# Kernel tuning notes

Measured on AMD Instinct MI355X. Metric: run time of the kernel, lower is better.

The kernel has to match this reference:

```python
import jax, jax.numpy as jnp
import numpy as np

N_NODES = 131072
N_EDGES = 1048576
D_IN, D_HID, D_OUT = 64, 64, 3
NUM_GRAPHS = 32


def setup_inputs() -> dict:
    key = jax.random.key(0)
    k = jax.random.split(key, 6)
    x = jax.random.normal(k[0], (N_NODES, D_IN), dtype=jnp.float32)
    edge_index = jax.random.randint(k[1], (2, N_EDGES), 0, N_NODES, dtype=jnp.int64)
    # batch assignment: 32 graphs of 4096 contiguous nodes each
    batch = jnp.repeat(jnp.arange(NUM_GRAPHS, dtype=jnp.int32), N_NODES // NUM_GRAPHS)
    W1 = jax.random.normal(k[2], (D_IN, D_HID), dtype=jnp.float32) * (1.0 / np.sqrt(D_IN))
    b1 = jnp.zeros((D_HID,), dtype=jnp.float32)
    W2 = jax.random.normal(k[3], (D_HID, D_OUT), dtype=jnp.float32) * (1.0 / np.sqrt(D_HID))
    b2 = jnp.zeros((D_OUT,), dtype=jnp.float32)
    return {"x": x, "edge_index": edge_index, "batch": batch,
            "W1": W1, "b1": b1, "W2": W2, "b2": b2}


def _gcn_conv(x, W, b, row, col, deg_inv_sqrt):
    # PyG GCNConv: x' = D^{-1/2}(A+I)D^{-1/2} X W + b (self-loops added)
    h = x @ W  # [N, d_out]
    norm = deg_inv_sqrt[row] * deg_inv_sqrt[col]  # [E]
    msg = h[row] * norm[:, None]                  # gather + scale
    agg = jax.ops.segment_sum(msg, col, num_segments=x.shape[0])
    # self-loop contribution: norm_ii = deg_inv_sqrt[i]^2
    agg = agg + h * (deg_inv_sqrt * deg_inv_sqrt)[:, None]
    return agg + b


def reference(x, edge_index, batch, W1, b1, W2, b2):
    N = x.shape[0]
    row, col = edge_index[0], edge_index[1]
    # degree at target nodes, including self-loops (+1)
    ones = jnp.ones((row.shape[0],), dtype=x.dtype)
    deg = jax.ops.segment_sum(ones, col, num_segments=N) + 1.0
    deg_inv_sqrt = jax.lax.rsqrt(deg)

    h = _gcn_conv(x, W1, b1, row, col, deg_inv_sqrt)
    h = jax.nn.relu(h)
    # F.dropout in eval mode is identity
    h = _gcn_conv(h, W2, b2, row, col, deg_inv_sqrt)

    # global_mean_pool over batch vector
    batch = batch.astype(jnp.int32)
    sums = jax.ops.segment_sum(h, batch, num_segments=NUM_GRAPHS)
    counts = jax.ops.segment_sum(jnp.ones((N,), dtype=h.dtype), batch, num_segments=NUM_GRAPHS)
    return sums / jnp.maximum(counts, 1.0)[:, None]
```

## Files before the change

### kernel.cpp

```cpp
#include <hip/hip_runtime.h>

#define NN 131072
#define NE 1048576
#define DD 64
#define NG 32
#define NPG 4096
#define NB 512
#define CAPB 2560
#define SCB 512

typedef __attribute__((ext_vector_type(2))) float f32x2;

extern "C" __global__ __launch_bounds__(256) void k_scgemm(
    const int* __restrict__ row, const int* __restrict__ col, int* __restrict__ bcursor,
    int* __restrict__ ebuf, const float* __restrict__ x, const float* __restrict__ W1,
    unsigned char* __restrict__ h1f, const float* __restrict__ b2, float* __restrict__ out) {
  __shared__ float4 wl[DD * 16];
  int t = threadIdx.x;
  if (blockIdx.x < SCB) {
    int* sh = reinterpret_cast<int*>(wl);
    int* sb = sh + NB;
    sh[t] = 0; sh[t + 256] = 0;
    __syncthreads();
    const int4* c4 = reinterpret_cast<const int4*>(col + blockIdx.x * 2048 + t * 8);
    int4 ca = c4[0], cb = c4[1];
    int cols[8] = {ca.x, ca.y, ca.z, ca.w, cb.x, cb.y, cb.z, cb.w};
    int lr[8];
#pragma unroll
    for (int k = 0; k < 8; ++k) lr[k] = atomicAdd(&sh[cols[k] >> 8], 1);
    __syncthreads();
    int h0 = sh[t];
    sb[t] = t * CAPB + (h0 ? atomicAdd(&bcursor[t], h0) : 0);
    int h1 = sh[t + 256];
    sb[t + 256] = (t + 256) * CAPB + (h1 ? atomicAdd(&bcursor[t + 256], h1) : 0);
    __syncthreads();
    const int4* r4 = reinterpret_cast<const int4*>(row + blockIdx.x * 2048 + t * 8);
    int4 ra = r4[0], rb = r4[1];
    int rows[8] = {ra.x, ra.y, ra.z, ra.w, rb.x, rb.y, rb.z, rb.w};
#pragma unroll
    for (int k = 0; k < 8; ++k) {
      int key = cols[k] >> 8;
      int pos = sb[key] + lr[k];
      if (pos < (key + 1) * CAPB)
        ebuf[pos] = (rows[k] << 8) | (cols[k] & 255);
    }
  } else {
    int gb = blockIdx.x - SCB;
    if (gb == 0 && t < NG * 3) out[t] = b2[t % 3];
    for (int i = t; i < DD * 16; i += 256) wl[i] = reinterpret_cast<const float4*>(W1)[i];
    __syncthreads();
    int jc = t & 3;
    int rg = t >> 2;
    size_t rbase = (size_t)gb * 128 + (size_t)rg * 2;
    const float4* xp = reinterpret_cast<const float4*>(x + rbase * DD);
    float4 acc[2][4];
#pragma unroll
    for (int r = 0; r < 2; ++r)
#pragma unroll
      for (int j = 0; j < 4; ++j) acc[r][j] = make_float4(0.f, 0.f, 0.f, 0.f);
#pragma unroll 2
    for (int kk = 0; kk < 16; ++kk) {
      float4 a0 = xp[kk];
      float4 a1 = xp[16 + kk];
#pragma unroll
      for (int j = 0; j < 4; ++j) {
        float4 w0 = wl[(4 * kk + 0) * 16 + jc * 4 + j];
        float4 w1 = wl[(4 * kk + 1) * 16 + jc * 4 + j];
        float4 w2 = wl[(4 * kk + 2) * 16 + jc * 4 + j];
        float4 w3 = wl[(4 * kk + 3) * 16 + jc * 4 + j];
        acc[0][j].x += a0.x * w0.x + a0.y * w1.x + a0.z * w2.x + a0.w * w3.x;
        acc[0][j].y += a0.x * w0.y + a0.y * w1.y + a0.z * w2.y + a0.w * w3.y;
        acc[0][j].z += a0.x * w0.z + a0.y * w1.z + a0.z * w2.z + a0.w * w3.z;
        acc[0][j].w += a0.x * w0.w + a0.y * w1.w + a0.z * w2.w + a0.w * w3.w;
        acc[1][j].x += a1.x * w0.x + a1.y * w1.x + a1.z * w2.x + a1.w * w3.x;
        acc[1][j].y += a1.x * w0.y + a1.y * w1.y + a1.z * w2.y + a1.w * w3.y;
        acc[1][j].z += a1.x * w0.z + a1.y * w1.z + a1.z * w2.z + a1.w * w3.z;
        acc[1][j].w += a1.x * w0.w + a1.y * w1.w + a1.z * w2.w + a1.w * w3.w;
      }
    }
#pragma unroll
    for (int r = 0; r < 2; ++r) {
      unsigned int d[4];
#pragma unroll
      for (int j = 0; j < 4; ++j) {
        float4 a = acc[r][j];
        int dj = __builtin_amdgcn_cvt_pk_fp8_f32(a.x, a.y, 0, false);
        dj = __builtin_amdgcn_cvt_pk_fp8_f32(a.z, a.w, dj, true);
        d[j] = (unsigned int)dj;
      }
      *reinterpret_cast<uint4*>(h1f + (rbase + r) * 64 + jc * 16) =
          make_uint4(d[0], d[1], d[2], d[3]);
    }
  }
}

extern "C" __global__ __launch_bounds__(256) void k_blocal(
    const int* __restrict__ ebuf, const int* __restrict__ bcursor, int* __restrict__ cnt,
    float* __restrict__ dis, int* __restrict__ starts, int* __restrict__ nbr) {
  __shared__ int sh[256];
  __shared__ int sx[256];
  int b = blockIdx.x, t = threadIdx.x;
  int bs = b * CAPB;
  int n_e = bcursor[b];
  if (n_e > CAPB) n_e = CAPB;
  sh[t] = 0;
  __syncthreads();
  for (int i = t; i < n_e; i += 256) atomicAdd(&sh[ebuf[bs + i] & 255], 1);
  __syncthreads();
  int v = sh[t];
  sx[t] = v;
  __syncthreads();
  for (int off = 1; off < 256; off <<= 1) {
    int u = (t >= off) ? sx[t - off] : 0;
    __syncthreads();
    sx[t] += u;
    __syncthreads();
  }
  int st = bs + sx[t] - v;
  int node = b * 256 + t;
  cnt[node] = v;
  dis[node] = rsqrtf((float)v + 1.0f);
  starts[node] = st;
  sx[t] = st;
  __syncthreads();
  for (int i = t; i < n_e; i += 256) {
    int ed = ebuf[bs + i];
    int pos = atomicAdd(&sx[ed & 255], 1);
    nbr[pos] = ed >> 8;
  }
}

extern "C" __global__ __launch_bounds__(256) void k_agg1f(
    const unsigned char* __restrict__ h1f, const int* __restrict__ starts,
    const int* __restrict__ cnt, const int* __restrict__ nbr, const float* __restrict__ dis,
    const float* __restrict__ b1, const float* __restrict__ W2, float4* __restrict__ h2) {
  __shared__ int2 sed[4][4][16];
  int lane = threadIdx.x & 63;
  int wid = threadIdx.x >> 6;
  int g = lane >> 4;
  int sl = lane & 15;
  int node = blockIdx.x * 16 + wid * 4 + g;
  int start = starts[node];
  int deg = cnt[node];
  float dc = dis[node];
  int2 s = make_int2(node, 0);
  if (sl < deg) {
    int nb = nbr[start + sl];
    s = make_int2(nb, __float_as_int(dis[nb] * dc));
  } else if (sl == deg) {
    s = make_int2(node, __float_as_int(dc * dc));
  }
  sed[wid][g][sl] = s;
  int m = (deg < 16) ? (deg + 1) : 16;
  int mw = max(m, __shfl_xor(m, 16));
  mw = max(mw, __shfl_xor(mw, 32));
  int mw8 = (mw + 7) & ~7;
  asm volatile("s_waitcnt lgkmcnt(0)" ::: "memory");
  __builtin_amdgcn_sched_barrier(0);
  const unsigned int* h1u = reinterpret_cast<const unsigned int*>(h1f);
  const int2* sp = sed[wid][g];
  float a0 = 0.f, a1 = 0.f, a2 = 0.f, a3 = 0.f;
  for (int e = 0; e < mw8; e += 8) {
    int2 e0 = sp[e + 0], e1 = sp[e + 1], e2 = sp[e + 2], e3 = sp[e + 3];
    int2 e4 = sp[e + 4], e5 = sp[e + 5], e6 = sp[e + 6], e7 = sp[e + 7];
    unsigned int u0 = h1u[(size_t)e0.x * 16 + sl];
    unsigned int u1 = h1u[(size_t)e1.x * 16 + sl];
    unsigned int u2 = h1u[(size_t)e2.x * 16 + sl];
    unsigned int u3 = h1u[(size_t)e3.x * 16 + sl];
    unsigned int u4 = h1u[(size_t)e4.x * 16 + sl];
    unsigned int u5 = h1u[(size_t)e5.x * 16 + sl];
    unsigned int u6 = h1u[(size_t)e6.x * 16 + sl];
    unsigned int u7 = h1u[(size_t)e7.x * 16 + sl];
    float w0 = __int_as_float(e0.y), w1 = __int_as_float(e1.y);
    float w2 = __int_as_float(e2.y), w3 = __int_as_float(e3.y);
    float w4 = __int_as_float(e4.y), w5 = __int_as_float(e5.y);
    float w6 = __int_as_float(e6.y), w7 = __int_as_float(e7.y);
    f32x2 p0 = __builtin_amdgcn_cvt_pk_f32_fp8(u0, false);
    f32x2 q0 = __builtin_amdgcn_cvt_pk_f32_fp8(u0, true);
    f32x2 p1 = __builtin_amdgcn_cvt_pk_f32_fp8(u1, false);
    f32x2 q1 = __builtin_amdgcn_cvt_pk_f32_fp8(u1, true);
    f32x2 p2 = __builtin_amdgcn_cvt_pk_f32_fp8(u2, false);
    f32x2 q2 = __builtin_amdgcn_cvt_pk_f32_fp8(u2, true);
    f32x2 p3 = __builtin_amdgcn_cvt_pk_f32_fp8(u3, false);
    f32x2 q3 = __builtin_amdgcn_cvt_pk_f32_fp8(u3, true);
    f32x2 p4 = __builtin_amdgcn_cvt_pk_f32_fp8(u4, false);
    f32x2 q4 = __builtin_amdgcn_cvt_pk_f32_fp8(u4, true);
    f32x2 p5 = __builtin_amdgcn_cvt_pk_f32_fp8(u5, false);
    f32x2 q5 = __builtin_amdgcn_cvt_pk_f32_fp8(u5, true);
    f32x2 p6 = __builtin_amdgcn_cvt_pk_f32_fp8(u6, false);
    f32x2 q6 = __builtin_amdgcn_cvt_pk_f32_fp8(u6, true);
    f32x2 p7 = __builtin_amdgcn_cvt_pk_f32_fp8(u7, false);
    f32x2 q7 = __builtin_amdgcn_cvt_pk_f32_fp8(u7, true);
    a0 = fmaf(w0, p0.x, a0); a1 = fmaf(w0, p0.y, a1); a2 = fmaf(w0, q0.x, a2); a3 = fmaf(w0, q0.y, a3);
    a0 = fmaf(w1, p1.x, a0); a1 = fmaf(w1, p1.y, a1); a2 = fmaf(w1, q1.x, a2); a3 = fmaf(w1, q1.y, a3);
    a0 = fmaf(w2, p2.x, a0); a1 = fmaf(w2, p2.y, a1); a2 = fmaf(w2, q2.x, a2); a3 = fmaf(w2, q2.y, a3);
    a0 = fmaf(w3, p3.x, a0); a1 = fmaf(w3, p3.y, a1); a2 = fmaf(w3, q3.x, a2); a3 = fmaf(w3, q3.y, a3);
    a0 = fmaf(w4, p4.x, a0); a1 = fmaf(w4, p4.y, a1); a2 = fmaf(w4, q4.x, a2); a3 = fmaf(w4, q4.y, a3);
    a0 = fmaf(w5, p5.x, a0); a1 = fmaf(w5, p5.y, a1); a2 = fmaf(w5, q5.x, a2); a3 = fmaf(w5, q5.y, a3);
    a0 = fmaf(w6, p6.x, a0); a1 = fmaf(w6, p6.y, a1); a2 = fmaf(w6, q6.x, a2); a3 = fmaf(w6, q6.y, a3);
    a0 = fmaf(w7, p7.x, a0); a1 = fmaf(w7, p7.y, a1); a2 = fmaf(w7, q7.x, a2); a3 = fmaf(w7, q7.y, a3);
  }
  if (deg >= 16) {
    for (int eo = 16; eo < deg; ++eo) {
      int r = nbr[start + eo];
      float q = dis[r] * dc;
      unsigned int u = h1u[(size_t)r * 16 + sl];
      f32x2 p = __builtin_amdgcn_cvt_pk_f32_fp8(u, false);
      f32x2 qq = __builtin_amdgcn_cvt_pk_f32_fp8(u, true);
      a0 = fmaf(q, p.x, a0); a1 = fmaf(q, p.y, a1);
      a2 = fmaf(q, qq.x, a2); a3 = fmaf(q, qq.y, a3);
    }
    float q = dc * dc;
    unsigned int u = h1u[(size_t)node * 16 + sl];
    f32x2 p = __builtin_amdgcn_cvt_pk_f32_fp8(u, false);
    f32x2 qq = __builtin_amdgcn_cvt_pk_f32_fp8(u, true);
    a0 = fmaf(q, p.x, a0); a1 = fmaf(q, p.y, a1);
    a2 = fmaf(q, qq.x, a2); a3 = fmaf(q, qq.y, a3);
  }
  float4 bb = *reinterpret_cast<const float4*>(b1 + 4 * sl);
  float z0 = fmaxf(a0 + bb.x, 0.f);
  float z1 = fmaxf(a1 + bb.y, 0.f);
  float z2 = fmaxf(a2 + bb.z, 0.f);
  float z3 = fmaxf(a3 + bb.w, 0.f);
  const float4* wp = reinterpret_cast<const float4*>(W2 + 12 * sl);
  float4 wA = wp[0];
  float4 wB = wp[1];
  float4 wC = wp[2];
  float v0 = z0 * wA.x + z1 * wA.w + z2 * wB.z + z3 * wC.y;
  float v1 = z0 * wA.y + z1 * wB.x + z2 * wB.w + z3 * wC.z;
  float v2 = z0 * wA.z + z1 * wB.y + z2 * wC.x + z3 * wC.w;
#pragma unroll
  for (int off = 8; off > 0; off >>= 1) {
    v0 += __shfl_xor(v0, off);
    v1 += __shfl_xor(v1, off);
    v2 += __shfl_xor(v2, off);
  }
  if (sl == 0) h2[node] = make_float4(v0 * dc, v1 * dc, v2 * dc, dc);
}

extern "C" __global__ __launch_bounds__(256) void k_agg2pool(
    const float4* __restrict__ h2, const int* __restrict__ starts, const int* __restrict__ cnt,
    const int* __restrict__ nbr, float* __restrict__ out) {
  int n = blockIdx.x * 256 + threadIdx.x;
  int start = starts[n], deg = cnt[n], end = start + deg;
  float4 hs = h2[n];
  float s0 = hs.x, s1 = hs.y, s2 = hs.z;
  int e = start;
  for (; e + 4 <= end; e += 4) {
    int n0 = nbr[e], n1 = nbr[e + 1], n2 = nbr[e + 2], n3 = nbr[e + 3];
    float4 h0 = h2[n0], h1 = h2[n1], g2 = h2[n2], g3 = h2[n3];
    s0 += (h0.x + h1.x) + (g2.x + g3.x);
    s1 += (h0.y + h1.y) + (g2.y + g3.y);
    s2 += (h0.z + h1.z) + (g2.z + g3.z);
  }
  for (; e < end; ++e) {
    float4 h0 = h2[nbr[e]];
    s0 += h0.x;
    s1 += h0.y;
    s2 += h0.z;
  }
  float dn = hs.w;
  s0 *= dn; s1 *= dn; s2 *= dn;
  __shared__ float red[3][256];
  int t = threadIdx.x;
  red[0][t] = s0; red[1][t] = s1; red[2][t] = s2;
  __syncthreads();
  for (int off = 128; off > 0; off >>= 1) {
    if (t < off) {
      red[0][t] += red[0][t + off];
      red[1][t] += red[1][t + off];
      red[2][t] += red[2][t + off];
    }
    __syncthreads();
  }
  if (t == 0) {
    int g = blockIdx.x >> 4;
    const float inv = 1.0f / (float)NPG;
    atomicAdd(&out[g * 3 + 0], red[0][0] * inv);
    atomicAdd(&out[g * 3 + 1], red[1][0] * inv);
    atomicAdd(&out[g * 3 + 2], red[2][0] * inv);
  }
}

extern "C" void kernel_launch(void* const* d_in, const int* in_sizes, int n_in,
                              void* d_out, int out_size, void* d_ws, size_t ws_size,
                              hipStream_t stream) {
  const float* x  = (const float*)d_in[0];
  const int*   ei = (const int*)d_in[1];
  const float* W1 = (const float*)d_in[3];
  const float* b1 = (const float*)d_in[4];
  const float* W2 = (const float*)d_in[5];
  const float* b2 = (const float*)d_in[6];
  const int* row = ei;
  const int* col = ei + NE;
  float* out = (float*)d_out;

  char* ws = (char*)d_ws;
  int*   cnt     = (int*)(ws + 0);
  float* dis     = (float*)(ws + (1u << 19));
  int*   starts  = (int*)(ws + (2u << 19));
  int*   bcursor = (int*)(ws + (3u << 19));
  int*   ebuf    = (int*)(ws + (4u << 19));
  int*   nbr     = (int*)(ws + (1u << 23));
  unsigned char* h1f = (unsigned char*)(ws + (1u << 24));
  float4* h2     = (float4*)(ws + (1u << 25) + 4096u);

  hipMemsetAsync(bcursor, 0, NB * sizeof(int), stream);
  k_scgemm<<<SCB + NN / 128, 256, 0, stream>>>(row, col, bcursor, ebuf, x, W1, h1f, b2, out);
  k_blocal<<<NB, 256, 0, stream>>>(ebuf, bcursor, cnt, dis, starts, nbr);
  k_agg1f<<<NN / 16, 256, 0, stream>>>(h1f, starts, cnt, nbr, dis, b1, W2, h2);
  k_agg2pool<<<NN / 256, 256, 0, stream>>>(h2, starts, cnt, nbr, out);
}
```

Measured before the change: 91.71 us.

## Split fused scatter/GEMM kernel, cache edges in LDS, two threads per node in pool

Splits the fused scatter+GEMM launch into a separate bucket-scatter kernel that handles 16 edges per thread and a standalone GEMM kernel that computes 4 rows per thread. The local bucket sort now keeps edges in shared memory so ebuf is read from global memory only once. The final aggregation+pool kernel assigns two threads per node, interleaving edges and combining them with a shuffle, to expose more memory parallelism. The cost is an extra kernel launch and the loss of the scatter/GEMM overlap the fused launch provided, plus higher register pressure in the GEMM.

```diff
diff --git a/kernel.cpp b/kernel.cpp
--- a/kernel.cpp
+++ b/kernel.cpp
@@ -7,96 +7,48 @@
 #define NPG 4096
 #define NB 512
 #define CAPB 2560
-#define SCB 512
 
 typedef __attribute__((ext_vector_type(2))) float f32x2;
 
-extern "C" __global__ __launch_bounds__(256) void k_scgemm(
+extern "C" __global__ __launch_bounds__(256) void k_bscatter(
     const int* __restrict__ row, const int* __restrict__ col, int* __restrict__ bcursor,
-    int* __restrict__ ebuf, const float* __restrict__ x, const float* __restrict__ W1,
-    unsigned char* __restrict__ h1f, const float* __restrict__ b2, float* __restrict__ out) {
-  __shared__ float4 wl[DD * 16];
+    int* __restrict__ ebuf) {
+  __shared__ int sh[NB];
+  __shared__ int sb[NB];
   int t = threadIdx.x;
-  if (blockIdx.x < SCB) {
-    int* sh = reinterpret_cast<int*>(wl);
-    int* sb = sh + NB;
-    sh[t] = 0; sh[t + 256] = 0;
-    __syncthreads();
-    const int4* c4 = reinterpret_cast<const int4*>(col + blockIdx.x * 2048 + t * 8);
-    int4 ca = c4[0], cb = c4[1];
-    int cols[8] = {ca.x, ca.y, ca.z, ca.w, cb.x, cb.y, cb.z, cb.w};
-    int lr[8];
-#pragma unroll
-    for (int k = 0; k < 8; ++k) lr[k] = atomicAdd(&sh[cols[k] >> 8], 1);
-    __syncthreads();
-    int h0 = sh[t];
-    sb[t] = t * CAPB + (h0 ? atomicAdd(&bcursor[t], h0) : 0);
-    int h1 = sh[t + 256];
-    sb[t + 256] = (t + 256) * CAPB + (h1 ? atomicAdd(&bcursor[t + 256], h1) : 0);
-    __syncthreads();
-    const int4* r4 = reinterpret_cast<const int4*>(row + blockIdx.x * 2048 + t * 8);
-    int4 ra = r4[0], rb = r4[1];
-    int rows[8] = {ra.x, ra.y, ra.z, ra.w, rb.x, rb.y, rb.z, rb.w};
-#pragma unroll
-    for (int k = 0; k < 8; ++k) {
-      int key = cols[k] >> 8;
-      int pos = sb[key] + lr[k];
-      if (pos < (key + 1) * CAPB)
-        ebuf[pos] = (rows[k] << 8) | (cols[k] & 255);
-    }
-  } else {
-    int gb = blockIdx.x - SCB;
-    if (gb == 0 && t < NG * 3) out[t] = b2[t % 3];
-    for (int i = t; i < DD * 16; i += 256) wl[i] = reinterpret_cast<const float4*>(W1)[i];
-    __syncthreads();
-    int jc = t & 3;
-    int rg = t >> 2;
-    size_t rbase = (size_t)gb * 128 + (size_t)rg * 2;
-    const float4* xp = reinterpret_cast<const float4*>(x + rbase * DD);
-    float4 acc[2][4];
-#pragma unroll
-    for (int r = 0; r < 2; ++r)
-#pragma unroll
-      for (int j = 0; j < 4; ++j) acc[r][j] = make_float4(0.f, 0.f, 0.f, 0.f);
-#pragma unroll 2
-    for (int kk = 0; kk < 16; ++kk) {
-      float4 a0 = xp[kk];
-      float4 a1 = xp[16 + kk];
-#pragma unroll
-      for (int j = 0; j < 4; ++j) {
-        float4 w0 = wl[(4 * kk + 0) * 16 + jc * 4 + j];
-        float4 w1 = wl[(4 * kk + 1) * 16 + jc * 4 + j];
-        float4 w2 = wl[(4 * kk + 2) * 16 + jc * 4 + j];
-        float4 w3 = wl[(4 * kk + 3) * 16 + jc * 4 + j];
-        acc[0][j].x += a0.x * w0.x + a0.y * w1.x + a0.z * w2.x + a0.w * w3.x;
-        acc[0][j].y += a0.x * w0.y + a0.y * w1.y + a0.z * w2.y + a0.w * w3.y;
-        acc[0][j].z += a0.x * w0.z + a0.y * w1.z + a0.z * w2.z + a0.w * w3.z;
-        acc[0][j].w += a0.x * w0.w + a0.y * w1.w + a0.z * w2.w + a0.w * w3.w;
-        acc[1][j].x += a1.x * w0.x + a1.y * w1.x + a1.z * w2.x + a1.w * w3.x;
-        acc[1][j].y += a1.x * w0.y + a1.y * w1.y + a1.z * w2.y + a1.w * w3.y;
-        acc[1][j].z += a1.x * w0.z + a1.y * w1.z + a1.z * w2.z + a1.w * w3.z;
-        acc[1][j].w += a1.x * w0.w + a1.y * w1.w + a1.z * w2.w + a1.w * w3.w;
-      }
-    }
-#pragma unroll
-    for (int r = 0; r < 2; ++r) {
-      unsigned int d[4];
-#pragma unroll
-      for (int j = 0; j < 4; ++j) {
-        float4 a = acc[r][j];
-        int dj = __builtin_amdgcn_cvt_pk_fp8_f32(a.x, a.y, 0, false);
-        dj = __builtin_amdgcn_cvt_pk_fp8_f32(a.z, a.w, dj, true);
-        d[j] = (unsigned int)dj;
-      }
-      *reinterpret_cast<uint4*>(h1f + (rbase + r) * 64 + jc * 16) =
-          make_uint4(d[0], d[1], d[2], d[3]);
-    }
+  sh[t] = 0; sh[t + 256] = 0;
+  __syncthreads();
+  int base = blockIdx.x * 4096 + t * 16;
+  const int4* c4 = reinterpret_cast<const int4*>(col + base);
+  int4 cA = c4[0], cB = c4[1], cC = c4[2], cD = c4[3];
+  int cols[16] = {cA.x, cA.y, cA.z, cA.w, cB.x, cB.y, cB.z, cB.w,
+                  cC.x, cC.y, cC.z, cC.w, cD.x, cD.y, cD.z, cD.w};
+  int lr[16];
+#pragma unroll
+  for (int k = 0; k < 16; ++k) lr[k] = atomicAdd(&sh[cols[k] >> 8], 1);
+  __syncthreads();
+  int h0 = sh[t];
+  sb[t] = t * CAPB + (h0 ? atomicAdd(&bcursor[t], h0) : 0);
+  int h1 = sh[t + 256];
+  sb[t + 256] = (t + 256) * CAPB + (h1 ? atomicAdd(&bcursor[t + 256], h1) : 0);
+  __syncthreads();
+  const int4* r4 = reinterpret_cast<const int4*>(row + base);
+  int4 rA = r4[0], rB = r4[1], rC = r4[2], rD = r4[3];
+  int rows[16] = {rA.x, rA.y, rA.z, rA.w, rB.x, rB.y, rB.z, rB.w,
+                  rC.x, rC.y, rC.z, rC.w, rD.x, rD.y, rD.z, rD.w};
+#pragma unroll
+  for (int k = 0; k < 16; ++k) {
+    int key = cols[k] >> 8;
+    int pos = sb[key] + lr[k];
+    if (pos < (key + 1) * CAPB)
+      ebuf[pos] = (rows[k] << 8) | (cols[k] & 255);
   }
 }
 
 extern "C" __global__ __launch_bounds__(256) void k_blocal(
     const int* __restrict__ ebuf, const int* __restrict__ bcursor, int* __restrict__ cnt,
     float* __restrict__ dis, int* __restrict__ starts, int* __restrict__ nbr) {
+  __shared__ int led[CAPB];
   __shared__ int sh[256];
   __shared__ int sx[256];
   int b = blockIdx.x, t = threadIdx.x;
@@ -105,7 +57,11 @@
   if (n_e > CAPB) n_e = CAPB;
   sh[t] = 0;
   __syncthreads();
-  for (int i = t; i < n_e; i += 256) atomicAdd(&sh[ebuf[bs + i] & 255], 1);
+  for (int i = t; i < n_e; i += 256) {
+    int ed = ebuf[bs + i];
+    led[i] = ed;
+    atomicAdd(&sh[ed & 255], 1);
+  }
   __syncthreads();
   int v = sh[t];
   sx[t] = v;
@@ -124,9 +80,71 @@
   sx[t] = st;
   __syncthreads();
   for (int i = t; i < n_e; i += 256) {
-    int ed = ebuf[bs + i];
+    int ed = led[i];
     int pos = atomicAdd(&sx[ed & 255], 1);
     nbr[pos] = ed >> 8;
+  }
+}
+
+extern "C" __global__ __launch_bounds__(256) void k_gemm1s(
+    const float* __restrict__ x, const float* __restrict__ W1,
+    unsigned char* __restrict__ h1f, const float* __restrict__ b2, float* __restrict__ out) {
+  __shared__ float4 wl[DD * 16];
+  int t = threadIdx.x;
+  if (blockIdx.x == 0 && t < NG * 3) out[t] = b2[t % 3];
+  for (int i = t; i < DD * 16; i += 256) wl[i] = reinterpret_cast<const float4*>(W1)[i];
+  __syncthreads();
+  int jc = t & 3;
+  int rg = t >> 2;
+  size_t rbase = (size_t)blockIdx.x * 256 + (size_t)rg * 4;
+  const float4* xp = reinterpret_cast<const float4*>(x + rbase * DD);
+  float4 acc[4][4];
+#pragma unroll
+  for (int r = 0; r < 4; ++r)
+#pragma unroll
+    for (int j = 0; j < 4; ++j) acc[r][j] = make_float4(0.f, 0.f, 0.f, 0.f);
+#pragma unroll 2
+  for (int kk = 0; kk < 16; ++kk) {
+    float4 a0 = xp[kk];
+    float4 a1 = xp[16 + kk];
+    float4 a2 = xp[32 + kk];
+    float4 a3 = xp[48 + kk];
+#pragma unroll
+    for (int j = 0; j < 4; ++j) {
+      float4 w0 = wl[(4 * kk + 0) * 16 + jc * 4 + j];
+      float4 w1 = wl[(4 * kk + 1) * 16 + jc * 4 + j];
+      float4 w2 = wl[(4 * kk + 2) * 16 + jc * 4 + j];
+      float4 w3 = wl[(4 * kk + 3) * 16 + jc * 4 + j];
+      acc[0][j].x += a0.x * w0.x + a0.y * w1.x + a0.z * w2.x + a0.w * w3.x;
+      acc[0][j].y += a0.x * w0.y + a0.y * w1.y + a0.z * w2.y + a0.w * w3.y;
+      acc[0][j].z += a0.x * w0.z + a0.y * w1.z + a0.z * w2.z + a0.w * w3.z;
+      acc[0][j].w += a0.x * w0.w + a0.y * w1.w + a0.z * w2.w + a0.w * w3.w;
+      acc[1][j].x += a1.x * w0.x + a1.y * w1.x + a1.z * w2.x + a1.w * w3.x;
+      acc[1][j].y += a1.x * w0.y + a1.y * w1.y + a1.z * w2.y + a1.w * w3.y;
+      acc[1][j].z += a1.x * w0.z + a1.y * w1.z + a1.z * w2.z + a1.w * w3.z;
+      acc[1][j].w += a1.x * w0.w + a1.y * w1.w + a1.z * w2.w + a1.w * w3.w;
+      acc[2][j].x += a2.x * w0.x + a2.y * w1.x + a2.z * w2.x + a2.w * w3.x;
+      acc[2][j].y += a2.x * w0.y + a2.y * w1.y + a2.z * w2.y + a2.w * w3.y;
+      acc[2][j].z += a2.x * w0.z + a2.y * w1.z + a2.z * w2.z + a2.w * w3.z;
+      acc[2][j].w += a2.x * w0.w + a2.y * w1.w + a2.z * w2.w + a2.w * w3.w;
+      acc[3][j].x += a3.x * w0.x + a3.y * w1.x + a3.z * w2.x + a3.w * w3.x;
+      acc[3][j].y += a3.x * w0.y + a3.y * w1.y + a3.z * w2.y + a3.w * w3.y;
+      acc[3][j].z += a3.x * w0.z + a3.y * w1.z + a3.z * w2.z + a3.w * w3.z;
+      acc[3][j].w += a3.x * w0.w + a3.y * w1.w + a3.z * w2.w + a3.w * w3.w;
+    }
+  }
+#pragma unroll
+  for (int r = 0; r < 4; ++r) {
+    unsigned int d[4];
+#pragma unroll
+    for (int j = 0; j < 4; ++j) {
+      float4 a = acc[r][j];
+      int dj = __builtin_amdgcn_cvt_pk_fp8_f32(a.x, a.y, 0, false);
+      dj = __builtin_amdgcn_cvt_pk_fp8_f32(a.z, a.w, dj, true);
+      d[j] = (unsigned int)dj;
+    }
+    *reinterpret_cast<uint4*>(h1f + (rbase + r) * 64 + jc * 16) =
+        make_uint4(d[0], d[1], d[2], d[3]);
   }
 }
 
@@ -241,26 +259,33 @@
 extern "C" __global__ __launch_bounds__(256) void k_agg2pool(
     const float4* __restrict__ h2, const int* __restrict__ starts, const int* __restrict__ cnt,
     const int* __restrict__ nbr, float* __restrict__ out) {
-  int n = blockIdx.x * 256 + threadIdx.x;
+  int gid = blockIdx.x * 256 + threadIdx.x;
+  int n = gid >> 1;
+  int par = gid & 1;
   int start = starts[n], deg = cnt[n], end = start + deg;
   float4 hs = h2[n];
-  float s0 = hs.x, s1 = hs.y, s2 = hs.z;
-  int e = start;
-  for (; e + 4 <= end; e += 4) {
-    int n0 = nbr[e], n1 = nbr[e + 1], n2 = nbr[e + 2], n3 = nbr[e + 3];
-    float4 h0 = h2[n0], h1 = h2[n1], g2 = h2[n2], g3 = h2[n3];
-    s0 += (h0.x + h1.x) + (g2.x + g3.x);
-    s1 += (h0.y + h1.y) + (g2.y + g3.y);
-    s2 += (h0.z + h1.z) + (g2.z + g3.z);
-  }
-  for (; e < end; ++e) {
+  float s0 = 0.f, s1 = 0.f, s2 = 0.f;
+  if (par == 0) { s0 = hs.x; s1 = hs.y; s2 = hs.z; }
+  int e = start + par;
+  for (; e + 2 < end; e += 4) {
+    int n0 = nbr[e], n1 = nbr[e + 2];
+    float4 h0 = h2[n0], h1 = h2[n1];
+    s0 += h0.x + h1.x;
+    s1 += h0.y + h1.y;
+    s2 += h0.z + h1.z;
+  }
+  for (; e < end; e += 2) {
     float4 h0 = h2[nbr[e]];
     s0 += h0.x;
     s1 += h0.y;
     s2 += h0.z;
   }
+  s0 += __shfl_xor(s0, 1);
+  s1 += __shfl_xor(s1, 1);
+  s2 += __shfl_xor(s2, 1);
   float dn = hs.w;
-  s0 *= dn; s1 *= dn; s2 *= dn;
+  if (par) { s0 = 0.f; s1 = 0.f; s2 = 0.f; }
+  else { s0 *= dn; s1 *= dn; s2 *= dn; }
   __shared__ float red[3][256];
   int t = threadIdx.x;
   red[0][t] = s0; red[1][t] = s1; red[2][t] = s2;
@@ -274,7 +299,7 @@
     __syncthreads();
   }
   if (t == 0) {
-    int g = blockIdx.x >> 4;
+    int g = blockIdx.x >> 5;
     const float inv = 1.0f / (float)NPG;
     atomicAdd(&out[g * 3 + 0], red[0][0] * inv);
     atomicAdd(&out[g * 3 + 1], red[1][0] * inv);
@@ -306,8 +331,9 @@
   float4* h2     = (float4*)(ws + (1u << 25) + 4096u);
 
   hipMemsetAsync(bcursor, 0, NB * sizeof(int), stream);
-  k_scgemm<<<SCB + NN / 128, 256, 0, stream>>>(row, col, bcursor, ebuf, x, W1, h1f, b2, out);
+  k_bscatter<<<NE / 4096, 256, 0, stream>>>(row, col, bcursor, ebuf);
   k_blocal<<<NB, 256, 0, stream>>>(ebuf, bcursor, cnt, dis, starts, nbr);
+  k_gemm1s<<<NN / 256, 256, 0, stream>>>(x, W1, h1f, b2, out);
   k_agg1f<<<NN / 16, 256, 0, stream>>>(h1f, starts, cnt, nbr, dis, b1, W2, h2);
-  k_agg2pool<<<NN / 256, 256, 0, stream>>>(h2, starts, cnt, nbr, out);
-}
+  k_agg2pool<<<NN * 2 / 256, 256, 0, stream>>>(h2, starts, cnt, nbr, out);
+}
```

Measured after the change: 95.80 us. 4.5% more time.
